# Kernel tuning notes

Measured on AMD Instinct MI355X. Metric: run time of the kernel, lower is better.

## Reference

```python
import jax, jax.numpy as jnp
import numpy as np

B, S, D = 2, 2048, 2048
H, HD = 16, 128          # num_heads, head_dim (H*HD == D)
I = 4096                 # intermediate_size; ffn in-dim is 2*I
EPS = 1e-5


def rmsnorm(x, w):
    return x * jax.lax.rsqrt(jnp.mean(x * x, axis=-1, keepdims=True) + EPS) * w


def setup_inputs() -> dict:
    key = jax.random.key(0)
    ks = jax.random.split(key, 12)
    sd = 0.02
    return {
        "hidden_states": jax.random.normal(ks[0], (B, S, D), jnp.float32),
        "attention_mask": jnp.zeros((B, S), jnp.float32),  # additive mask
        "rn1_w": jnp.ones((D,), jnp.float32),
        "wq": jax.random.normal(ks[1], (D, D), jnp.float32) * sd,
        "wk": jax.random.normal(ks[2], (D, D), jnp.float32) * sd,
        "wv": jax.random.normal(ks[3], (D, D), jnp.float32) * sd,
        "wo": jax.random.normal(ks[4], (D, D), jnp.float32) * sd,
        "rn2_w": jnp.ones((D,), jnp.float32),
        "w1": jax.random.normal(ks[5], (D, 2 * I), jnp.float32) * sd,      # Linear(d, 2*I, bias=False)
        "fc1_w": jax.random.normal(ks[6], (2 * I, I), jnp.float32) * sd,   # SwiGLU fc1
        "fc1_b": jnp.zeros((I,), jnp.float32),
        "fc2_w": jax.random.normal(ks[7], (2 * I, I), jnp.float32) * sd,   # SwiGLU fc2
        "fc2_b": jnp.zeros((I,), jnp.float32),
        "w3": jax.random.normal(ks[8], (I, D), jnp.float32) * sd,          # Linear(I, d, bias=False)
    }


def reference(hidden_states, attention_mask, rn1_w, wq, wk, wv, wo, rn2_w,
              w1, fc1_w, fc1_b, fc2_w, fc2_b, w3):
    # --- attention ---
    attn_in = rmsnorm(hidden_states, rn1_w)
    q = (attn_in @ wq).reshape(B, S, H, HD)
    k = (attn_in @ wk).reshape(B, S, H, HD)
    v = (attn_in @ wv).reshape(B, S, H, HD)
    # rope_cache is None -> no rotary embedding applied
    scores = jnp.einsum("bqhd,bkhd->bhqk", q, k) / np.sqrt(HD).astype(np.float32)
    scores = scores + attention_mask[:, None, None, :]  # [B,1,1,S] broadcast
    probs = jax.nn.softmax(scores, axis=-1)             # dropout p=0 (eval)
    attn = jnp.einsum("bhqk,bkhd->bqhd", probs, v).reshape(B, S, D)
    residual1 = hidden_states + attn @ wo
    # --- SwiGLU FFN ---
    ffn_in = rmsnorm(residual1, rn2_w)
    x = ffn_in @ w1                                      # [B,S,2I]
    gated = jax.nn.silu(x @ fc1_w + fc1_b) * (x @ fc2_w + fc2_b)  # [B,S,I]
    return residual1 + gated @ w3
```

## Files before the change

kernel.cpp:

```cpp
#include <hip/hip_runtime.h>
#include <hip/hip_bf16.h>
#include <stdint.h>

using short8 = __attribute__((ext_vector_type(8))) short;
using f32x4  = __attribute__((ext_vector_type(4))) float;

#define DEV __device__ __forceinline__

DEV float b2f(unsigned short u) {
  union { unsigned int i; float f; } v; v.i = ((unsigned int)u) << 16; return v.f;
}
DEV unsigned short f2b(float f) {
  union { float f; unsigned int i; } v; v.f = f;
  unsigned int x = v.i;
  return (unsigned short)((x + 0x7FFFu + ((x >> 16) & 1u)) >> 16);
}
DEV void g2lds16(const void* g, void* l) {
  __builtin_amdgcn_global_load_lds((const __attribute__((address_space(1))) void*)g,
                                   (__attribute__((address_space(3))) void*)l, 16, 0, 0);
}

enum { EPI_BF16 = 0, EPI_RESID_F32 = 1, EPI_BIAS_BF16 = 2, EPI_RESID_OUT = 3 };

template<int EPI>
__global__ __launch_bounds__(512, 2)
void gemm_bt256(const unsigned short* __restrict__ A, const unsigned short* __restrict__ Bt,
                void* __restrict__ Cout, const void* __restrict__ extra,
                int M, int N, int K) {
  __shared__ __align__(16) unsigned short As[2][256 * 64];
  __shared__ __align__(16) unsigned short Bs[2][256 * 64];
  const int nbx = N >> 8;
  int wg = blockIdx.x;
  const int nwg = gridDim.x;
  if ((nwg & 7) == 0) wg = (wg & 7) * (nwg >> 3) + (wg >> 3);
  const int by = wg / nbx, bx = wg % nbx;
  const int m0 = by << 8, n0 = bx << 8;
  const int t = threadIdx.x;
  const int l = t & 63, wid = t >> 6;
  const int lr = l & 15, lg = l >> 4;
  const int wr = (wid >> 2) << 7;
  const int wc = (wid & 3) << 6;

  f32x4 acc[8][4];
#pragma unroll
  for (int i = 0; i < 8; ++i)
#pragma unroll
    for (int j = 0; j < 4; ++j) acc[i][j] = (f32x4){0.f, 0.f, 0.f, 0.f};

  const int sr = t >> 3;
  const int scSwz = ((t & 7) << 3) ^ ((sr & 7) << 3);
  const unsigned short* Ag = A  + (size_t)(m0 + sr) * K + scSwz;
  const unsigned short* Bg = Bt + (size_t)(n0 + sr) * K + scSwz;
  const int nT = K >> 6;

  auto stageA = [&](int tt) {
    unsigned short* dst = &As[tt & 1][t * 8];
    const unsigned short* src = Ag + ((size_t)tt << 6);
#pragma unroll
    for (int ld = 0; ld < 4; ++ld) g2lds16(src + (size_t)(ld * 64) * K, dst + ld * 4096);
  };
  auto stageB = [&](int tt) {
    unsigned short* dst = &Bs[tt & 1][t * 8];
    const unsigned short* src = Bg + ((size_t)tt << 6);
#pragma unroll
    for (int ld = 0; ld < 4; ++ld) g2lds16(src + (size_t)(ld * 64) * K, dst + ld * 4096);
  };

  const int xorv = (lr & 7) << 3;
  const int cb0 = (lg * 8) ^ xorv;
  const int cb1 = (32 + lg * 8) ^ xorv;

  short8 afA[2][2], afB[2][2], bfr[4][2];

#define READ_A(dst, base, p)                                          \
  {                                                                   \
    const int ro0 = (wr + ((p) * 2 + 0) * 16 + lr) << 6;              \
    const int ro1 = (wr + ((p) * 2 + 1) * 16 + lr) << 6;              \
    dst[0][0] = *(const short8*)((base) + ro0 + cb0);                 \
    dst[0][1] = *(const short8*)((base) + ro0 + cb1);                 \
    dst[1][0] = *(const short8*)((base) + ro1 + cb0);                 \
    dst[1][1] = *(const short8*)((base) + ro1 + cb1);                 \
  }
#define READ_B(base)                                                  \
  {                                                                   \
    _Pragma("unroll")                                                 \
    for (int ni = 0; ni < 4; ++ni) {                                  \
      const int ro = (wc + ni * 16 + lr) << 6;                        \
      bfr[ni][0] = *(const short8*)((base) + ro + cb0);               \
      bfr[ni][1] = *(const short8*)((base) + ro + cb1);               \
    }                                                                 \
  }
#define MFMA_PH(af, r0)                                               \
  {                                                                   \
    _Pragma("unroll")                                                 \
    for (int kk = 0; kk < 2; ++kk)                                    \
      _Pragma("unroll")                                               \
      for (int a = 0; a < 2; ++a)                                     \
        _Pragma("unroll")                                             \
        for (int ni = 0; ni < 4; ++ni)                                \
          acc[(r0) + a][ni] = __builtin_amdgcn_mfma_f32_16x16x32_bf16(\
              af[a][kk], bfr[ni][kk], acc[(r0) + a][ni], 0, 0, 0);    \
  }

  stageA(0); stageB(0);
  asm volatile("s_waitcnt vmcnt(0)\n\ts_barrier" ::: "memory");
  {
    const unsigned short* base = &As[0][0];
    const unsigned short* bbase = &Bs[0][0];
    READ_A(afA, base, 0);
    READ_B(bbase);
  }

  for (int tt = 0; tt < nT; ++tt) {
    const unsigned short* base = &As[tt & 1][0];
    const bool more = (tt + 1) < nT;
    READ_A(afB, base, 1);
    if (more) stageA(tt + 1);
    asm volatile("s_waitcnt lgkmcnt(4)" ::: "memory");
    __builtin_amdgcn_sched_barrier(0);
    __builtin_amdgcn_s_setprio(1);
    MFMA_PH(afA, 0);
    __builtin_amdgcn_s_setprio(0);
    asm volatile("s_barrier" ::: "memory");
    READ_A(afA, base, 2);
    if (more) stageB(tt + 1);
    asm volatile("s_waitcnt lgkmcnt(4)" ::: "memory");
    __builtin_amdgcn_sched_barrier(0);
    __builtin_amdgcn_s_setprio(1);
    MFMA_PH(afB, 2);
    __builtin_amdgcn_s_setprio(0);
    asm volatile("s_barrier" ::: "memory");
    READ_A(afB, base, 3);
    asm volatile("s_waitcnt lgkmcnt(4)" ::: "memory");
    __builtin_amdgcn_sched_barrier(0);
    __builtin_amdgcn_s_setprio(1);
    MFMA_PH(afA, 4);
    __builtin_amdgcn_s_setprio(0);
    asm volatile("s_barrier" ::: "memory");
    asm volatile("s_waitcnt lgkmcnt(0)" ::: "memory");
    __builtin_amdgcn_sched_barrier(0);
    __builtin_amdgcn_s_setprio(1);
    MFMA_PH(afB, 6);
    __builtin_amdgcn_s_setprio(0);
    asm volatile("s_waitcnt vmcnt(0)\n\ts_barrier" ::: "memory");
    if (more) {
      const unsigned short* nbase = &As[(tt + 1) & 1][0];
      const unsigned short* nbbase = &Bs[(tt + 1) & 1][0];
      READ_A(afA, nbase, 0);
      READ_B(nbbase);
    }
  }
#undef READ_A
#undef READ_B
#undef MFMA_PH

#pragma unroll
  for (int mi = 0; mi < 8; ++mi) {
#pragma unroll
    for (int ni = 0; ni < 4; ++ni) {
      const int col = n0 + wc + ni * 16 + lr;
#pragma unroll
      for (int j = 0; j < 4; ++j) {
        const int row = m0 + wr + mi * 16 + lg * 4 + j;
        const size_t idx = (size_t)row * N + col;
        const float v = acc[mi][ni][j];
        if constexpr (EPI == EPI_BF16) {
          ((unsigned short*)Cout)[idx] = f2b(v);
        } else if constexpr (EPI == EPI_RESID_F32) {
          ((float*)Cout)[idx] = v + ((const float*)extra)[idx];
        } else if constexpr (EPI == EPI_BIAS_BF16) {
          ((unsigned short*)Cout)[idx] = f2b(v + ((const float*)extra)[col]);
        } else {
          ((float*)Cout)[idx] = v + ((const float*)extra)[idx];
        }
      }
    }
  }
}

template<int EPI>
__global__ __launch_bounds__(256)
void gemm_bt(const unsigned short* __restrict__ A, const unsigned short* __restrict__ Bt,
             void* __restrict__ Cout, const void* __restrict__ extra,
             int M, int N, int K) {
  __shared__ __align__(16) unsigned short As[128 * 64];
  __shared__ __align__(16) unsigned short Bs[128 * 64];
  const int nbx = N >> 7;
  int wg = blockIdx.x;
  const int nwg = gridDim.x;
  if ((nwg & 7) == 0) wg = (wg & 7) * (nwg >> 3) + (wg >> 3);
  const int by = wg / nbx, bx = wg % nbx;
  const int m0 = by << 7, n0 = bx << 7;
  const int t = threadIdx.x;
  const int l = t & 63, w = t >> 6;
  const int lr = l & 15, lg = l >> 4;
  const int wr = (w >> 1) << 6, wc = (w & 1) << 6;

  f32x4 acc[4][4];
#pragma unroll
  for (int i = 0; i < 4; ++i)
#pragma unroll
    for (int j = 0; j < 4; ++j) acc[i][j] = (f32x4){0.f, 0.f, 0.f, 0.f};

  const int sr = t >> 3;
  const int skSwz = ((t & 7) << 3) ^ ((sr & 7) << 3);
  const unsigned short* Ag = A  + (size_t)(m0 + sr) * K + skSwz;
  const unsigned short* Bg = Bt + (size_t)(n0 + sr) * K + skSwz;
  unsigned short* Al = As + t * 8;
  unsigned short* Bl = Bs + t * 8;

  for (int kt = 0; kt < K; kt += 64) {
#pragma unroll
    for (int c = 0; c < 4; ++c) {
      g2lds16(Ag + (size_t)(c * 32) * K + kt, Al + c * 2048);
      g2lds16(Bg + (size_t)(c * 32) * K + kt, Bl + c * 2048);
    }
    __syncthreads();
#pragma unroll
    for (int ks = 0; ks < 2; ++ks) {
      short8 af[4], bfr[4];
#pragma unroll
      for (int mi = 0; mi < 4; ++mi) {
        const int row = wr + mi * 16 + lr;
        af[mi] = *(const short8*)(As + (row << 6) + (((ks * 32 + lg * 8)) ^ ((row & 7) << 3)));
      }
#pragma unroll
      for (int ni = 0; ni < 4; ++ni) {
        const int row = wc + ni * 16 + lr;
        bfr[ni] = *(const short8*)(Bs + (row << 6) + (((ks * 32 + lg * 8)) ^ ((row & 7) << 3)));
      }
#pragma unroll
      for (int mi = 0; mi < 4; ++mi)
#pragma unroll
        for (int ni = 0; ni < 4; ++ni)
          acc[mi][ni] = __builtin_amdgcn_mfma_f32_16x16x32_bf16(af[mi], bfr[ni], acc[mi][ni], 0, 0, 0);
    }
    __syncthreads();
  }

#pragma unroll
  for (int mi = 0; mi < 4; ++mi) {
#pragma unroll
    for (int ni = 0; ni < 4; ++ni) {
      const int col = n0 + wc + ni * 16 + lr;
#pragma unroll
      for (int j = 0; j < 4; ++j) {
        const int row = m0 + wr + mi * 16 + lg * 4 + j;
        const size_t idx = (size_t)row * N + col;
        const float v = acc[mi][ni][j];
        if constexpr (EPI == EPI_BF16) {
          ((unsigned short*)Cout)[idx] = f2b(v);
        } else if constexpr (EPI == EPI_RESID_F32) {
          ((float*)Cout)[idx] = v + ((const float*)extra)[idx];
        } else if constexpr (EPI == EPI_BIAS_BF16) {
          ((unsigned short*)Cout)[idx] = f2b(v + ((const float*)extra)[col]);
        } else {
          ((float*)Cout)[idx] = v + ((const float*)extra)[idx];
        }
      }
    }
  }
}

__global__ __launch_bounds__(256)
void attn_fwd(const unsigned short* __restrict__ qkv, const unsigned short* __restrict__ vt,
              const float* __restrict__ mask, unsigned short* __restrict__ out) {
  __shared__ __align__(16) unsigned short Ks[64 * 128];
  __shared__ __align__(16) unsigned short Vs[128 * 64];
  __shared__ __align__(16) unsigned short Ps[4][16 * 64];
  const int b = blockIdx.z, hh = blockIdx.y;
  const int q0 = blockIdx.x << 6;
  const int t = threadIdx.x, l = t & 63, w = t >> 6;
  const int lr = l & 15, lg = l >> 4;
  const float scale = 0.08838834764831845f;

  short8 qf[4];
  {
    const unsigned short* qb = qkv + (size_t)(b * 2048 + q0 + w * 16 + lr) * 6144 + hh * 128;
#pragma unroll
    for (int ks = 0; ks < 4; ++ks) qf[ks] = *(const short8*)(qb + ks * 32 + lg * 8);
  }
  f32x4 acc_o[8];
#pragma unroll
  for (int i = 0; i < 8; ++i) acc_o[i] = (f32x4){0.f, 0.f, 0.f, 0.f};
  float m_r[4], l_r[4];
#pragma unroll
  for (int j = 0; j < 4; ++j) { m_r[j] = -1e30f; l_r[j] = 0.f; }

  const unsigned short* kb = qkv + (size_t)(b * 2048) * 6144 + 2048 + hh * 128;
  const unsigned short* vb = vt + (size_t)(b * 16 + hh) * 128 * 2048;
  const float* mb = mask + b * 2048;

  for (int kt = 0; kt < 2048; kt += 64) {
#pragma unroll
    for (int c = 0; c < 4; ++c) {
      const int e = (c * 256 + t) * 8;
      const int kr = e >> 7, kc = e & 127;
      g2lds16(kb + (size_t)(kt + kr) * 6144 + (kc ^ ((kr & 7) << 3)), Ks + e);
      const int vr = e >> 6, vc = e & 63;
      g2lds16(vb + (size_t)vr * 2048 + kt + (vc ^ ((vr & 7) << 3)), Vs + e);
    }
    __syncthreads();

    f32x4 sc[4];
#pragma unroll
    for (int nt = 0; nt < 4; ++nt) {
      f32x4 s = (f32x4){0.f, 0.f, 0.f, 0.f};
#pragma unroll
      for (int ks = 0; ks < 4; ++ks) {
        short8 kf = *(const short8*)(Ks + ((nt * 16 + lr) << 7) + ((ks * 32 + lg * 8) ^ ((lr & 7) << 3)));
        s = __builtin_amdgcn_mfma_f32_16x16x32_bf16(qf[ks], kf, s, 0, 0, 0);
      }
      sc[nt] = s;
    }
#pragma unroll
    for (int nt = 0; nt < 4; ++nt) {
      const float mv = mb[kt + nt * 16 + lr];
#pragma unroll
      for (int j = 0; j < 4; ++j) sc[nt][j] = sc[nt][j] * scale + mv;
    }
#pragma unroll
    for (int j = 0; j < 4; ++j) {
      float tm = fmaxf(fmaxf(sc[0][j], sc[1][j]), fmaxf(sc[2][j], sc[3][j]));
      tm = fmaxf(tm, __shfl_xor(tm, 1));
      tm = fmaxf(tm, __shfl_xor(tm, 2));
      tm = fmaxf(tm, __shfl_xor(tm, 4));
      tm = fmaxf(tm, __shfl_xor(tm, 8));
      const float mn = fmaxf(m_r[j], tm);
      const float corr = __expf(m_r[j] - mn);
      m_r[j] = mn;
      float ps = 0.f;
#pragma unroll
      for (int nt = 0; nt < 4; ++nt) {
        const float p = __expf(sc[nt][j] - mn);
        sc[nt][j] = p;
        ps += p;
      }
      ps += __shfl_xor(ps, 1);
      ps += __shfl_xor(ps, 2);
      ps += __shfl_xor(ps, 4);
      ps += __shfl_xor(ps, 8);
      l_r[j] = l_r[j] * corr + ps;
#pragma unroll
      for (int di = 0; di < 8; ++di) acc_o[di][j] *= corr;
    }
#pragma unroll
    for (int nt = 0; nt < 4; ++nt)
#pragma unroll
      for (int j = 0; j < 4; ++j) {
        const int q = lg * 4 + j;
        Ps[w][(q << 6) + ((nt * 16 + lr) ^ ((q & 7) << 3))] = f2b(sc[nt][j]);
      }
    asm volatile("s_waitcnt lgkmcnt(0)" ::: "memory");
#pragma unroll
    for (int ks2 = 0; ks2 < 2; ++ks2) {
      short8 pf = *(const short8*)(&Ps[w][(lr << 6) + ((ks2 * 32 + lg * 8) ^ ((lr & 7) << 3))]);
#pragma unroll
      for (int di = 0; di < 8; ++di) {
        short8 vf = *(const short8*)(Vs + ((di * 16 + lr) << 6) + ((ks2 * 32 + lg * 8) ^ ((lr & 7) << 3)));
        acc_o[di] = __builtin_amdgcn_mfma_f32_16x16x32_bf16(pf, vf, acc_o[di], 0, 0, 0);
      }
    }
    __syncthreads();
  }
#pragma unroll
  for (int di = 0; di < 8; ++di)
#pragma unroll
    for (int j = 0; j < 4; ++j) {
      const int q = q0 + w * 16 + lg * 4 + j;
      out[(size_t)(b * 2048 + q) * 2048 + hh * 128 + di * 16 + lr] = f2b(acc_o[di][j] / l_r[j]);
    }
}

__global__ __launch_bounds__(256)
void rmsnorm_k(const float* __restrict__ in, const float* __restrict__ wgt,
               unsigned short* __restrict__ out) {
  __shared__ float red[4];
  const int row = blockIdx.x, t = threadIdx.x;
  const float4* rp = (const float4*)(in + (size_t)row * 2048 + t * 8);
  float4 a = rp[0], b = rp[1];
  float x[8] = {a.x, a.y, a.z, a.w, b.x, b.y, b.z, b.w};
  float s = 0.f;
#pragma unroll
  for (int i = 0; i < 8; ++i) s += x[i] * x[i];
#pragma unroll
  for (int m = 1; m < 64; m <<= 1) s += __shfl_xor(s, m);
  const int l = t & 63, w = t >> 6;
  if (l == 0) red[w] = s;
  __syncthreads();
  const float tot = red[0] + red[1] + red[2] + red[3];
  const float rr = rsqrtf(tot * (1.f / 2048.f) + 1e-5f);
  const float4* wp = (const float4*)(wgt + t * 8);
  float4 wa = wp[0], wb = wp[1];
  float ww[8] = {wa.x, wa.y, wa.z, wa.w, wb.x, wb.y, wb.z, wb.w};
  short8 o;
#pragma unroll
  for (int i = 0; i < 8; ++i) o[i] = (short)f2b(x[i] * rr * ww[i]);
  *(short8*)(out + (size_t)row * 2048 + t * 8) = o;
}

__global__ __launch_bounds__(256)
void transpose2d(const float* __restrict__ in, unsigned short* __restrict__ out,
                 int R, int C) {
  __shared__ __align__(16) unsigned short tile[64][72];
  const int r0 = blockIdx.y << 6, c0 = blockIdx.x << 6;
  const int t = threadIdx.x;
#pragma unroll
  for (int it = 0; it < 4; ++it) {
    const int e = (it * 256 + t) * 4;
    const int r = e >> 6, cc = e & 63;
    float4 v = *(const float4*)(in + (size_t)(r0 + r) * C + c0 + cc);
    tile[cc + 0][r] = f2b(v.x);
    tile[cc + 1][r] = f2b(v.y);
    tile[cc + 2][r] = f2b(v.z);
    tile[cc + 3][r] = f2b(v.w);
  }
  __syncthreads();
#pragma unroll
  for (int it = 0; it < 2; ++it) {
    const int e = (it * 256 + t) * 8;
    const int rr = e >> 6, kk = e & 63;
    short8 v = *(const short8*)(&tile[rr][kk]);
    *(short8*)(out + (size_t)(c0 + rr) * R + r0 + kk) = v;
  }
}

__global__ __launch_bounds__(256)
void transpose_v(const unsigned short* __restrict__ qkv, unsigned short* __restrict__ vt) {
  __shared__ __align__(16) unsigned short tile[64][72];
  const int s0 = blockIdx.x << 6, d0 = blockIdx.y << 6;
  const int z = blockIdx.z;
  const unsigned short* in = qkv + (size_t)((z >> 4) * 2048) * 6144 + 4096 + (z & 15) * 128;
  unsigned short* outp = vt + (size_t)z * 128 * 2048;
  const int t = threadIdx.x;
#pragma unroll
  for (int it = 0; it < 2; ++it) {
    const int e = (it * 256 + t) * 8;
    const int r = e >> 6, cc = e & 63;
    short8 v = *(const short8*)(in + (size_t)(s0 + r) * 6144 + d0 + cc);
#pragma unroll
    for (int i = 0; i < 8; ++i) tile[cc + i][r] = (unsigned short)v[i];
  }
  __syncthreads();
#pragma unroll
  for (int it = 0; it < 2; ++it) {
    const int e = (it * 256 + t) * 8;
    const int rr = e >> 6, kk = e & 63;
    short8 v = *(const short8*)(&tile[rr][kk]);
    *(short8*)(outp + (size_t)(d0 + rr) * 2048 + s0 + kk) = v;
  }
}

__global__ __launch_bounds__(256)
void swiglu_k(const unsigned short* __restrict__ g1, const unsigned short* __restrict__ g2,
              unsigned short* __restrict__ gated) {
  const size_t i = ((size_t)blockIdx.x * 256 + threadIdx.x) * 8;
  short8 a = *(const short8*)(g1 + i);
  short8 b = *(const short8*)(g2 + i);
  short8 o;
#pragma unroll
  for (int j = 0; j < 8; ++j) {
    const float x = b2f((unsigned short)a[j]);
    const float y = b2f((unsigned short)b[j]);
    o[j] = (short)f2b(x / (1.f + __expf(-x)) * y);
  }
  *(short8*)(gated + i) = o;
}

extern "C" void kernel_launch(void* const* d_in, const int* in_sizes, int n_in,
                              void* d_out, int out_size, void* d_ws, size_t ws_size,
                              hipStream_t stream) {
  const float* h    = (const float*)d_in[0];
  const float* mask = (const float*)d_in[1];
  const float* rn1w = (const float*)d_in[2];
  const float* wq   = (const float*)d_in[3];
  const float* wk   = (const float*)d_in[4];
  const float* wv   = (const float*)d_in[5];
  const float* wo   = (const float*)d_in[6];
  const float* rn2w = (const float*)d_in[7];
  const float* w1   = (const float*)d_in[8];
  const float* fc1w = (const float*)d_in[9];
  const float* fc1b = (const float*)d_in[10];
  const float* fc2w = (const float*)d_in[11];
  const float* fc2b = (const float*)d_in[12];
  const float* w3   = (const float*)d_in[13];

  char* ws = (char*)d_ws;
  size_t off = 0;
  auto alloc = [&](size_t bytes) { char* p = ws + off; off += (bytes + 255) & ~(size_t)255; return p; };
  unsigned short* bufA = (unsigned short*)alloc(16777216);
  unsigned short* bufB = (unsigned short*)alloc(16777216);
  unsigned short* qkv  = (unsigned short*)alloc(50331648);
  float*          r1f  = (float*)alloc(33554432);
  unsigned short* xbuf = (unsigned short*)alloc(67108864);
  unsigned short* g1   = (unsigned short*)alloc(33554432);
  unsigned short* g2   = (unsigned short*)alloc(33554432);
  unsigned short* wt   = (unsigned short*)alloc(67108864);
  if (off > ws_size) return;

  rmsnorm_k<<<4096, 256, 0, stream>>>(h, rn1w, bufA);
  transpose2d<<<dim3(32, 32), 256, 0, stream>>>(wq, wt,                 2048, 2048);
  transpose2d<<<dim3(32, 32), 256, 0, stream>>>(wk, wt + 2048 * 2048,   2048, 2048);
  transpose2d<<<dim3(32, 32), 256, 0, stream>>>(wv, wt + 2 * 2048 * 2048, 2048, 2048);
  gemm_bt256<EPI_BF16><<<384, 512, 0, stream>>>(bufA, wt, qkv, nullptr, 4096, 6144, 2048);
  transpose_v<<<dim3(32, 2, 32), 256, 0, stream>>>(qkv, bufB);
  attn_fwd<<<dim3(32, 16, 2), 256, 0, stream>>>(qkv, bufB, mask, bufA);
  transpose2d<<<dim3(32, 32), 256, 0, stream>>>(wo, wt, 2048, 2048);
  gemm_bt<EPI_RESID_F32><<<512, 256, 0, stream>>>(bufA, wt, r1f, h, 4096, 2048, 2048);

  rmsnorm_k<<<4096, 256, 0, stream>>>(r1f, rn2w, bufB);
  transpose2d<<<dim3(128, 32), 256, 0, stream>>>(w1, wt, 2048, 8192);
  gemm_bt256<EPI_BF16><<<512, 512, 0, stream>>>(bufB, wt, xbuf, nullptr, 4096, 8192, 2048);
  transpose2d<<<dim3(64, 128), 256, 0, stream>>>(fc1w, wt, 8192, 4096);
  gemm_bt256<EPI_BIAS_BF16><<<256, 512, 0, stream>>>(xbuf, wt, g1, fc1b, 4096, 4096, 8192);
  transpose2d<<<dim3(64, 128), 256, 0, stream>>>(fc2w, wt, 8192, 4096);
  gemm_bt256<EPI_BIAS_BF16><<<256, 512, 0, stream>>>(xbuf, wt, g2, fc2b, 4096, 4096, 8192);
  unsigned short* gated = qkv;
  swiglu_k<<<8192, 256, 0, stream>>>(g1, g2, gated);
  transpose2d<<<dim3(32, 64), 256, 0, stream>>>(w3, wt, 4096, 2048);
  gemm_bt<EPI_RESID_OUT><<<512, 256, 0, stream>>>(gated, wt, d_out, r1f, 4096, 2048, 4096);
}
```

Measured before the change: 1.213 ms.

## Fuse SwiGLU into fc2 GEMM epilogue and pack bf16 pairs in transpose

```diff
diff --git a/kernel.cpp b/kernel.cpp
--- a/kernel.cpp
+++ b/kernel.cpp
@@ -3,6 +3,7 @@
 #include <stdint.h>
 
 using short8 = __attribute__((ext_vector_type(8))) short;
+using uint4v = __attribute__((ext_vector_type(4))) unsigned int;
 using f32x4  = __attribute__((ext_vector_type(4))) float;
 
 #define DEV __device__ __forceinline__
@@ -20,13 +21,13 @@
                                    (__attribute__((address_space(3))) void*)l, 16, 0, 0);
 }
 
-enum { EPI_BF16 = 0, EPI_RESID_F32 = 1, EPI_BIAS_BF16 = 2, EPI_RESID_OUT = 3 };
+enum { EPI_BF16 = 0, EPI_RESID_F32 = 1, EPI_BIAS_BF16 = 2, EPI_RESID_OUT = 3, EPI_SWIGLU = 4 };
 
 template<int EPI>
 __global__ __launch_bounds__(512, 2)
 void gemm_bt256(const unsigned short* __restrict__ A, const unsigned short* __restrict__ Bt,
                 void* __restrict__ Cout, const void* __restrict__ extra,
-                int M, int N, int K) {
+                const void* __restrict__ extra2, int M, int N, int K) {
   __shared__ __align__(16) unsigned short As[2][256 * 64];
   __shared__ __align__(16) unsigned short Bs[2][256 * 64];
   const int nbx = N >> 8;
@@ -53,18 +54,9 @@
   const unsigned short* Bg = Bt + (size_t)(n0 + sr) * K + scSwz;
   const int nT = K >> 6;
 
-  auto stageA = [&](int tt) {
-    unsigned short* dst = &As[tt & 1][t * 8];
-    const unsigned short* src = Ag + ((size_t)tt << 6);
-#pragma unroll
-    for (int ld = 0; ld < 4; ++ld) g2lds16(src + (size_t)(ld * 64) * K, dst + ld * 4096);
-  };
-  auto stageB = [&](int tt) {
-    unsigned short* dst = &Bs[tt & 1][t * 8];
-    const unsigned short* src = Bg + ((size_t)tt << 6);
-#pragma unroll
-    for (int ld = 0; ld < 4; ++ld) g2lds16(src + (size_t)(ld * 64) * K, dst + ld * 4096);
-  };
+  const unsigned short* AgNext = Ag + 64;
+  const unsigned short* BgNext = Bg + 64;
+  const size_t rowK64 = (size_t)64 * K;
 
   const int xorv = (lr & 7) << 3;
   const int cb0 = (lg * 8) ^ xorv;
@@ -72,6 +64,20 @@
 
   short8 afA[2][2], afB[2][2], bfr[4][2];
 
+#define STAGE_A(buf)                                                  \
+  {                                                                   \
+    unsigned short* dst = &As[buf][t * 8];                            \
+    _Pragma("unroll")                                                 \
+    for (int ld = 0; ld < 4; ++ld)                                    \
+      g2lds16(AgNext + (size_t)ld * rowK64, dst + ld * 4096);         \
+  }
+#define STAGE_B(buf)                                                  \
+  {                                                                   \
+    unsigned short* dst = &Bs[buf][t * 8];                            \
+    _Pragma("unroll")                                                 \
+    for (int ld = 0; ld < 4; ++ld)                                    \
+      g2lds16(BgNext + (size_t)ld * rowK64, dst + ld * 4096);         \
+  }
 #define READ_A(dst, base, p)                                          \
   {                                                                   \
     const int ro0 = (wr + ((p) * 2 + 0) * 16 + lr) << 6;              \
@@ -102,20 +108,25 @@
               af[a][kk], bfr[ni][kk], acc[(r0) + a][ni], 0, 0, 0);    \
   }
 
-  stageA(0); stageB(0);
+  {
+    unsigned short* dstA = &As[0][t * 8];
+    unsigned short* dstB = &Bs[0][t * 8];
+#pragma unroll
+    for (int ld = 0; ld < 4; ++ld) {
+      g2lds16(Ag + (size_t)ld * rowK64, dstA + ld * 4096);
+      g2lds16(Bg + (size_t)ld * rowK64, dstB + ld * 4096);
+    }
+  }
   asm volatile("s_waitcnt vmcnt(0)\n\ts_barrier" ::: "memory");
-  {
-    const unsigned short* base = &As[0][0];
-    const unsigned short* bbase = &Bs[0][0];
-    READ_A(afA, base, 0);
-    READ_B(bbase);
-  }
+  READ_A(afA, &As[0][0], 0);
+  READ_B(&Bs[0][0]);
 
   for (int tt = 0; tt < nT; ++tt) {
     const unsigned short* base = &As[tt & 1][0];
+    const int nb = (tt + 1) & 1;
     const bool more = (tt + 1) < nT;
     READ_A(afB, base, 1);
-    if (more) stageA(tt + 1);
+    if (more) STAGE_A(nb);
     asm volatile("s_waitcnt lgkmcnt(4)" ::: "memory");
     __builtin_amdgcn_sched_barrier(0);
     __builtin_amdgcn_s_setprio(1);
@@ -123,7 +134,7 @@
     __builtin_amdgcn_s_setprio(0);
     asm volatile("s_barrier" ::: "memory");
     READ_A(afA, base, 2);
-    if (more) stageB(tt + 1);
+    if (more) STAGE_B(nb);
     asm volatile("s_waitcnt lgkmcnt(4)" ::: "memory");
     __builtin_amdgcn_sched_barrier(0);
     __builtin_amdgcn_s_setprio(1);
@@ -144,12 +155,14 @@
     __builtin_amdgcn_s_setprio(0);
     asm volatile("s_waitcnt vmcnt(0)\n\ts_barrier" ::: "memory");
     if (more) {
-      const unsigned short* nbase = &As[(tt + 1) & 1][0];
-      const unsigned short* nbbase = &Bs[(tt + 1) & 1][0];
-      READ_A(afA, nbase, 0);
-      READ_B(nbbase);
-    }
-  }
+      AgNext += 64;
+      BgNext += 64;
+      READ_A(afA, &As[nb][0], 0);
+      READ_B(&Bs[nb][0]);
+    }
+  }
+#undef STAGE_A
+#undef STAGE_B
 #undef READ_A
 #undef READ_B
 #undef MFMA_PH
@@ -170,6 +183,10 @@
           ((float*)Cout)[idx] = v + ((const float*)extra)[idx];
         } else if constexpr (EPI == EPI_BIAS_BF16) {
           ((unsigned short*)Cout)[idx] = f2b(v + ((const float*)extra)[col]);
+        } else if constexpr (EPI == EPI_SWIGLU) {
+          const float g1v = b2f(((const unsigned short*)extra2)[idx]);
+          const float v2 = v + ((const float*)extra)[col];
+          ((unsigned short*)Cout)[idx] = f2b(g1v / (1.f + __expf(-g1v)) * v2);
         } else {
           ((float*)Cout)[idx] = v + ((const float*)extra)[idx];
         }
@@ -402,26 +419,36 @@
 __global__ __launch_bounds__(256)
 void transpose2d(const float* __restrict__ in, unsigned short* __restrict__ out,
                  int R, int C) {
-  __shared__ __align__(16) unsigned short tile[64][72];
+  __shared__ __align__(16) unsigned int tile2[64][36];
   const int r0 = blockIdx.y << 6, c0 = blockIdx.x << 6;
   const int t = threadIdx.x;
 #pragma unroll
-  for (int it = 0; it < 4; ++it) {
-    const int e = (it * 256 + t) * 4;
-    const int r = e >> 6, cc = e & 63;
-    float4 v = *(const float4*)(in + (size_t)(r0 + r) * C + c0 + cc);
-    tile[cc + 0][r] = f2b(v.x);
-    tile[cc + 1][r] = f2b(v.y);
-    tile[cc + 2][r] = f2b(v.z);
-    tile[cc + 3][r] = f2b(v.w);
+  for (int it = 0; it < 2; ++it) {
+    const int p = it * 256 + t;
+    const int r2 = p >> 4;
+    const int c = (p & 15) << 2;
+    const float* src = in + (size_t)(r0 + r2 * 2) * C + c0 + c;
+    float4 va = *(const float4*)(src);
+    float4 vb = *(const float4*)(src + C);
+    tile2[c + 0][r2] = (unsigned int)f2b(va.x) | ((unsigned int)f2b(vb.x) << 16);
+    tile2[c + 1][r2] = (unsigned int)f2b(va.y) | ((unsigned int)f2b(vb.y) << 16);
+    tile2[c + 2][r2] = (unsigned int)f2b(va.z) | ((unsigned int)f2b(vb.z) << 16);
+    tile2[c + 3][r2] = (unsigned int)f2b(va.w) | ((unsigned int)f2b(vb.w) << 16);
   }
   __syncthreads();
 #pragma unroll
   for (int it = 0; it < 2; ++it) {
-    const int e = (it * 256 + t) * 8;
-    const int rr = e >> 6, kk = e & 63;
-    short8 v = *(const short8*)(&tile[rr][kk]);
-    *(short8*)(out + (size_t)(c0 + rr) * R + r0 + kk) = v;
+    const int u = it * 256 + t;
+    const int rr = u >> 3;
+    const int k8 = u & 7;
+    uint4v v = *(const uint4v*)(&tile2[rr][k8 * 4]);
+    short8 o;
+#pragma unroll
+    for (int j = 0; j < 4; ++j) {
+      o[2 * j]     = (short)(v[j] & 0xFFFFu);
+      o[2 * j + 1] = (short)(v[j] >> 16);
+    }
+    *(short8*)(out + (size_t)(c0 + rr) * R + r0 + k8 * 8) = o;
   }
 }
 
@@ -449,22 +476,6 @@
     short8 v = *(const short8*)(&tile[rr][kk]);
     *(short8*)(outp + (size_t)(d0 + rr) * 2048 + s0 + kk) = v;
   }
-}
-
-__global__ __launch_bounds__(256)
-void swiglu_k(const unsigned short* __restrict__ g1, const unsigned short* __restrict__ g2,
-              unsigned short* __restrict__ gated) {
-  const size_t i = ((size_t)blockIdx.x * 256 + threadIdx.x) * 8;
-  short8 a = *(const short8*)(g1 + i);
-  short8 b = *(const short8*)(g2 + i);
-  short8 o;
-#pragma unroll
-  for (int j = 0; j < 8; ++j) {
-    const float x = b2f((unsigned short)a[j]);
-    const float y = b2f((unsigned short)b[j]);
-    o[j] = (short)f2b(x / (1.f + __expf(-x)) * y);
-  }
-  *(short8*)(gated + i) = o;
 }
 
 extern "C" void kernel_launch(void* const* d_in, const int* in_sizes, int n_in,
@@ -494,7 +505,6 @@
   float*          r1f  = (float*)alloc(33554432);
   unsigned short* xbuf = (unsigned short*)alloc(67108864);
   unsigned short* g1   = (unsigned short*)alloc(33554432);
-  unsigned short* g2   = (unsigned short*)alloc(33554432);
   unsigned short* wt   = (unsigned short*)alloc(67108864);
   if (off > ws_size) return;
 
@@ -502,7 +512,7 @@
   transpose2d<<<dim3(32, 32), 256, 0, stream>>>(wq, wt,                 2048, 2048);
   transpose2d<<<dim3(32, 32), 256, 0, stream>>>(wk, wt + 2048 * 2048,   2048, 2048);
   transpose2d<<<dim3(32, 32), 256, 0, stream>>>(wv, wt + 2 * 2048 * 2048, 2048, 2048);
-  gemm_bt256<EPI_BF16><<<384, 512, 0, stream>>>(bufA, wt, qkv, nullptr, 4096, 6144, 2048);
+  gemm_bt256<EPI_BF16><<<384, 512, 0, stream>>>(bufA, wt, qkv, nullptr, nullptr, 4096, 6144, 2048);
   transpose_v<<<dim3(32, 2, 32), 256, 0, stream>>>(qkv, bufB);
   attn_fwd<<<dim3(32, 16, 2), 256, 0, stream>>>(qkv, bufB, mask, bufA);
   transpose2d<<<dim3(32, 32), 256, 0, stream>>>(wo, wt, 2048, 2048);
@@ -510,13 +520,12 @@
 
   rmsnorm_k<<<4096, 256, 0, stream>>>(r1f, rn2w, bufB);
   transpose2d<<<dim3(128, 32), 256, 0, stream>>>(w1, wt, 2048, 8192);
-  gemm_bt256<EPI_BF16><<<512, 512, 0, stream>>>(bufB, wt, xbuf, nullptr, 4096, 8192, 2048);
+  gemm_bt256<EPI_BF16><<<512, 512, 0, stream>>>(bufB, wt, xbuf, nullptr, nullptr, 4096, 8192, 2048);
   transpose2d<<<dim3(64, 128), 256, 0, stream>>>(fc1w, wt, 8192, 4096);
-  gemm_bt256<EPI_BIAS_BF16><<<256, 512, 0, stream>>>(xbuf, wt, g1, fc1b, 4096, 4096, 8192);
+  gemm_bt256<EPI_BIAS_BF16><<<256, 512, 0, stream>>>(xbuf, wt, g1, fc1b, nullptr, 4096, 4096, 8192);
   transpose2d<<<dim3(64, 128), 256, 0, stream>>>(fc2w, wt, 8192, 4096);
-  gemm_bt256<EPI_BIAS_BF16><<<256, 512, 0, stream>>>(xbuf, wt, g2, fc2b, 4096, 4096, 8192);
   unsigned short* gated = qkv;
-  swiglu_k<<<8192, 256, 0, stream>>>(g1, g2, gated);
+  gemm_bt256<EPI_SWIGLU><<<256, 512, 0, stream>>>(xbuf, wt, gated, fc2b, g1, 4096, 4096, 8192);
   transpose2d<<<dim3(32, 64), 256, 0, stream>>>(w3, wt, 4096, 2048);
   gemm_bt<EPI_RESID_OUT><<<512, 256, 0, stream>>>(gated, wt, d_out, r1f, 4096, 2048, 4096);
 }
```

Measured after the change: 1.204 ms. Within noise of the previous version (-0.7%).
